# Optimization experiments

Measured on AMD Instinct MI355X. Metric: run time of the kernel, lower is better.

Reference implementation:

```python
import jax, jax.numpy as jnp
import numpy as np
import math

N, IN, OUT, H, EDIM, E = 50000, 128, 64, 2, 64, 1600000
HC = H * OUT
EPS = 1e-16


def segment_softmax(alpha, idx, num_segments):
    # alpha: [E, H], idx: [E] destination node per edge
    m = jax.ops.segment_max(alpha, idx, num_segments=num_segments)  # [N, H]
    m = jnp.where(jnp.isfinite(m), m, 0.0)
    a = jnp.exp(alpha - m[idx])
    s = jax.ops.segment_sum(a, idx, num_segments=num_segments)  # [N, H]
    return a / (s[idx] + EPS)


def setup_inputs() -> dict:
    key = jax.random.key(0)
    ks = jax.random.split(key, 10)
    sx = 1.0 / math.sqrt(IN)
    se = 1.0 / math.sqrt(EDIM)
    x = jax.random.normal(ks[0], (N, IN), dtype=jnp.float32)
    edge_index = jax.random.randint(ks[1], (2, E), 0, N, dtype=jnp.int64)
    edge_attr = jax.random.normal(ks[2], (E, EDIM), dtype=jnp.float32)
    Wq = jax.random.normal(ks[3], (IN, HC), dtype=jnp.float32) * sx
    bq = jnp.zeros((HC,), dtype=jnp.float32)
    Wk = jax.random.normal(ks[4], (IN, HC), dtype=jnp.float32) * sx
    bk = jnp.zeros((HC,), dtype=jnp.float32)
    Wv = jax.random.normal(ks[5], (IN, HC), dtype=jnp.float32) * sx
    bv = jnp.zeros((HC,), dtype=jnp.float32)
    We = jax.random.normal(ks[6], (EDIM, HC), dtype=jnp.float32) * se  # lin_edge, no bias
    Wskip = jax.random.normal(ks[7], (IN, HC), dtype=jnp.float32) * sx
    bskip = jnp.zeros((HC,), dtype=jnp.float32)
    return {"x": x, "edge_index": edge_index, "edge_attr": edge_attr,
            "Wq": Wq, "bq": bq, "Wk": Wk, "bk": bk, "Wv": Wv, "bv": bv,
            "We": We, "Wskip": Wskip, "bskip": bskip}


def reference(x, edge_index, edge_attr, Wq, bq, Wk, bk, Wv, bv, We, Wskip, bskip):
    src, dst = edge_index[0], edge_index[1]  # messages flow src(j) -> dst(i)
    q = (x @ Wq + bq).reshape(N, H, OUT)
    k = (x @ Wk + bk).reshape(N, H, OUT)
    v = (x @ Wv + bv).reshape(N, H, OUT)
    e = (edge_attr @ We).reshape(E, H, OUT)
    k_j = k[src] + e                      # [E, H, C]
    q_i = q[dst]                          # [E, H, C]
    alpha = jnp.sum(q_i * k_j, axis=-1) / math.sqrt(OUT)  # [E, H]
    alpha = segment_softmax(alpha, dst, N)                # dropout=identity (eval)
    msg = (v[src] + e) * alpha[:, :, None]                # [E, H, C]
    out = jax.ops.segment_sum(msg, dst, num_segments=N).reshape(N, HC)
    out = out + x @ Wskip + bskip          # root_weight skip connection
    return out
```

## Files before the change

kernel.cpp:

```cpp
#include <hip/hip_runtime.h>
#include <hip/hip_fp16.h>

constexpr int NN = 50000;
constexpr int EE = 1600000;
constexpr int NB = 196;

typedef __attribute__((ext_vector_type(8))) short bf16x8;
typedef __attribute__((ext_vector_type(4))) float f32x4;

__device__ inline short f2bf(float f) {
    unsigned u = __builtin_bit_cast(unsigned, f);
    u += 0x7fff + ((u >> 16) & 1);
    return (short)(u >> 16);
}

__global__ __launch_bounds__(256) void node_gemm(
    const float* __restrict__ x,
    const float* __restrict__ Wq, const float* __restrict__ bq,
    const float* __restrict__ Wk, const float* __restrict__ bk,
    const float* __restrict__ Wv, const float* __restrict__ bv,
    const float* __restrict__ Ws, const float* __restrict__ bs,
    __half* __restrict__ qt, __half* __restrict__ kt, __half* __restrict__ vt,
    float* __restrict__ skip)
{
    __shared__ short As[64 * 128];
    __shared__ short Bs[128 * 128];
    const int tid = threadIdx.x;
    const int mat = blockIdx.y;
    const float* __restrict__ W    = mat == 0 ? Wq : mat == 1 ? Wk : mat == 2 ? Wv : Ws;
    const float* __restrict__ bias = mat == 0 ? bq : mat == 1 ? bk : mat == 2 ? bv : bs;

    #pragma unroll 4
    for (int idx = tid; idx < 16384; idx += 256) {
        int k = idx >> 7, n = idx & 127;
        int chunk = (k >> 3) ^ (n & 15);
        Bs[n * 128 + chunk * 8 + (k & 7)] = f2bf(W[idx]);
    }
    const int row0 = blockIdx.x * 64;
    #pragma unroll 4
    for (int idx = tid; idx < 8192; idx += 256) {
        int r = idx >> 7, k = idx & 127;
        int node = row0 + r;
        float v = (node < NN) ? x[(size_t)node * 128 + k] : 0.f;
        int chunk = (k >> 3) ^ (r & 15);
        As[r * 128 + chunk * 8 + (k & 7)] = f2bf(v);
    }
    __syncthreads();

    const int wave = tid >> 6, lane = tid & 63;
    const int m16 = lane & 15, quad = lane >> 4;
    const int arow = wave * 16 + m16;
    f32x4 acc[8] = {};
    #pragma unroll
    for (int ks = 0; ks < 4; ks++) {
        int c = ks * 4 + quad;
        bf16x8 af = *(const bf16x8*)&As[arow * 128 + (c ^ (arow & 15)) * 8];
        #pragma unroll
        for (int t = 0; t < 8; t++) {
            int n = t * 16 + m16;
            bf16x8 bf = *(const bf16x8*)&Bs[n * 128 + (c ^ (n & 15)) * 8];
            acc[t] = __builtin_amdgcn_mfma_f32_16x16x32_bf16(af, bf, acc[t], 0, 0, 0);
        }
    }
    __half* __restrict__ T = mat == 0 ? qt : mat == 1 ? kt : vt;
    #pragma unroll
    for (int t = 0; t < 8; t++) {
        int col = t * 16 + m16;
        float bv_ = bias[col];
        #pragma unroll
        for (int r = 0; r < 4; r++) {
            int node = row0 + wave * 16 + quad * 4 + r;
            if (node < NN) {
                float val = acc[t][r] + bv_;
                if (mat < 3)
                    T[node * 128 + (col & 63) * 2 + (col >> 6)] = __float2half(val);
                else
                    skip[node * 128 + col] = val;
            }
        }
    }
}

__global__ __launch_bounds__(256) void edge_gemm(
    const float* __restrict__ ea, const float* __restrict__ We,
    __half* __restrict__ et)
{
    __shared__ short As[64 * 64];
    __shared__ short Bs[128 * 64];
    const int tid = threadIdx.x;
    #pragma unroll 4
    for (int idx = tid; idx < 8192; idx += 256) {
        int k = idx >> 7, n = idx & 127;
        int chunk = (k >> 3) ^ (n & 7);
        Bs[n * 64 + chunk * 8 + (k & 7)] = f2bf(We[idx]);
    }
    const int row0 = blockIdx.x * 64;
    #pragma unroll 4
    for (int idx = tid; idx < 4096; idx += 256) {
        int r = idx >> 6, k = idx & 63;
        int chunk = (k >> 3) ^ (r & 7);
        As[r * 64 + chunk * 8 + (k & 7)] = f2bf(ea[(size_t)(row0 + r) * 64 + k]);
    }
    __syncthreads();

    const int wave = tid >> 6, lane = tid & 63;
    const int m16 = lane & 15, quad = lane >> 4;
    const int arow = wave * 16 + m16;
    f32x4 acc[8] = {};
    #pragma unroll
    for (int ks = 0; ks < 2; ks++) {
        int c = ks * 4 + quad;
        bf16x8 af = *(const bf16x8*)&As[arow * 64 + (c ^ (arow & 7)) * 8];
        #pragma unroll
        for (int t = 0; t < 8; t++) {
            int n = t * 16 + m16;
            bf16x8 bf = *(const bf16x8*)&Bs[n * 64 + (c ^ (n & 7)) * 8];
            acc[t] = __builtin_amdgcn_mfma_f32_16x16x32_bf16(af, bf, acc[t], 0, 0, 0);
        }
    }
    #pragma unroll
    for (int t = 0; t < 8; t++) {
        int col = t * 16 + m16;
        int coff = (col & 63) * 2 + (col >> 6);
        #pragma unroll
        for (int r = 0; r < 4; r++) {
            int edge = row0 + wave * 16 + quad * 4 + r;
            et[(size_t)edge * 128 + coff] = __float2half(acc[t][r]);
        }
    }
}

__global__ void k_hist(const int* __restrict__ dst, int* __restrict__ cnt) {
    int i = blockIdx.x * 256 + threadIdx.x;
    if (i < EE) atomicAdd(&cnt[dst[i]], 1);
}

__global__ __launch_bounds__(256) void k_scan1(const int* __restrict__ cnt,
                                               int* __restrict__ offs,
                                               int* __restrict__ bsum) {
    __shared__ int s[256];
    int t = threadIdx.x, i = blockIdx.x * 256 + t;
    int v = (i < NN) ? cnt[i] : 0;
    s[t] = v; __syncthreads();
    #pragma unroll
    for (int d = 1; d < 256; d <<= 1) {
        int u = (t >= d) ? s[t - d] : 0;
        __syncthreads(); s[t] += u; __syncthreads();
    }
    if (i < NN) offs[i] = s[t] - v;
    if (t == 255) bsum[blockIdx.x] = s[255];
}

__global__ __launch_bounds__(256) void k_scan2(int* __restrict__ bsum) {
    __shared__ int s[256];
    int t = threadIdx.x;
    int v = (t < NB) ? bsum[t] : 0;
    s[t] = v; __syncthreads();
    #pragma unroll
    for (int d = 1; d < 256; d <<= 1) {
        int u = (t >= d) ? s[t - d] : 0;
        __syncthreads(); s[t] += u; __syncthreads();
    }
    if (t < NB) bsum[t] = s[t] - v;
}

__global__ void k_scan3(int* __restrict__ offs, const int* __restrict__ bsum) {
    int i = blockIdx.x * 256 + threadIdx.x;
    if (i < NN) offs[i] += bsum[i >> 8];
    if (i == NN) offs[NN] = EE;
}

__global__ void k_scatter(const int* __restrict__ ei, const int* __restrict__ offs,
                          int* __restrict__ curp, int2* __restrict__ sorted) {
    int i = blockIdx.x * 256 + threadIdx.x;
    if (i >= EE) return;
    int d = ei[EE + i];
    int pos = offs[d] + atomicAdd(&curp[d], 1);
    sorted[pos] = make_int2(ei[i], i);
}

__global__ __launch_bounds__(256) void k_edge(
    const __half2* __restrict__ qt, const __half2* __restrict__ kt,
    const __half2* __restrict__ vt, const __half2* __restrict__ et,
    const int2* __restrict__ sorted, const int* __restrict__ offs,
    const float* __restrict__ skip, float* __restrict__ out)
{
    const int node = blockIdx.x * 4 + (threadIdx.x >> 6);
    const int lane = threadIdx.x & 63;
    if (node >= NN) return;
    const float K2E = 1.4426950408889634f / 8.0f;

    float2 qf = __half22float2(qt[node * 64 + lane]);
    float s0 = 0.f, s1 = 0.f, a0 = 0.f, a1 = 0.f;
    const int beg = offs[node], end = offs[node + 1];

    for (int base = beg; base < end; base += 64) {
        int cnt = min(64, end - base);
        int2 myp = (lane < cnt) ? sorted[base + lane] : make_int2(0, 0);
        for (int i = 0; i < cnt; i++) {
            int src = __shfl(myp.x, i);
            int eid = __shfl(myp.y, i);
            float2 kf = __half22float2(kt[src * 64 + lane]);
            float2 vf = __half22float2(vt[src * 64 + lane]);
            float2 ef = __half22float2(et[(size_t)eid * 64 + lane]);
            float p0 = qf.x * (kf.x + ef.x);
            float p1 = qf.y * (kf.y + ef.y);
            #pragma unroll
            for (int m = 32; m; m >>= 1) {
                p0 += __shfl_xor(p0, m);
                p1 += __shfl_xor(p1, m);
            }
            float al0 = exp2f(p0 * K2E);
            float al1 = exp2f(p1 * K2E);
            s0 += al0; s1 += al1;
            a0 += al0 * (vf.x + ef.x);
            a1 += al1 * (vf.y + ef.y);
        }
    }
    float o0 = a0 / (s0 + 1e-16f) + skip[node * 128 + lane];
    float o1 = a1 / (s1 + 1e-16f) + skip[node * 128 + 64 + lane];
    out[node * 128 + lane] = o0;
    out[node * 128 + 64 + lane] = o1;
}

extern "C" void kernel_launch(void* const* d_in, const int* in_sizes, int n_in,
                              void* d_out, int out_size, void* d_ws, size_t ws_size,
                              hipStream_t stream) {
    const float* x   = (const float*)d_in[0];
    const int*   ei  = (const int*)d_in[1];
    const float* ea  = (const float*)d_in[2];
    const float* Wq  = (const float*)d_in[3];
    const float* bq  = (const float*)d_in[4];
    const float* Wk  = (const float*)d_in[5];
    const float* bk  = (const float*)d_in[6];
    const float* Wv  = (const float*)d_in[7];
    const float* bv  = (const float*)d_in[8];
    const float* We  = (const float*)d_in[9];
    const float* Wsk = (const float*)d_in[10];
    const float* bsk = (const float*)d_in[11];
    float* out = (float*)d_out;

    char* w = (char*)d_ws;
    __half* qt   = (__half*)(w + 0);
    __half* kt   = (__half*)(w + 12800000);
    __half* vt   = (__half*)(w + 25600000);
    float*  skip = (float*)(w + 38400000);
    __half* et   = (__half*)(w + 64000000);
    int2*   sorted = (int2*)(w + 473600000);
    int*    cnt  = (int*)(w + 486400000);
    int*    curp = (int*)(w + 486600000);
    int*    bsum = (int*)(w + 486800000);
    int*    offs = (int*)(w + 486801024);

    (void)hipMemsetAsync(w + 486400000, 0, 401024, stream);

    node_gemm<<<dim3(782, 4), 256, 0, stream>>>(x, Wq, bq, Wk, bk, Wv, bv, Wsk, bsk,
                                                qt, kt, vt, skip);
    edge_gemm<<<25000, 256, 0, stream>>>(ea, We, et);
    k_hist<<<6250, 256, 0, stream>>>(ei + EE, cnt);
    k_scan1<<<NB, 256, 0, stream>>>(cnt, offs, bsum);
    k_scan2<<<1, 256, 0, stream>>>(bsum);
    k_scan3<<<NB, 256, 0, stream>>>(offs, bsum);
    k_scatter<<<6250, 256, 0, stream>>>(ei, offs, curp, sorted);
    k_edge<<<12500, 256, 0, stream>>>((const __half2*)qt, (const __half2*)kt,
                                      (const __half2*)vt, (const __half2*)et,
                                      sorted, offs, skip, out);
}
```

Baseline: 1.168 ms.

## Pre-transpose weights to bf16, interleave K/V, and vectorize edge attention loop

Measured after the change: 1.061 ms. 9.1% less time.

```diff
diff --git a/kernel.cpp b/kernel.cpp
--- a/kernel.cpp
+++ b/kernel.cpp
@@ -7,6 +7,7 @@
 
 typedef __attribute__((ext_vector_type(8))) short bf16x8;
 typedef __attribute__((ext_vector_type(4))) float f32x4;
+typedef _Float16 half2v __attribute__((ext_vector_type(2)));
 
 __device__ inline short f2bf(float f) {
     unsigned u = __builtin_bit_cast(unsigned, f);
@@ -14,36 +15,71 @@
     return (short)(u >> 16);
 }
 
+__device__ inline float fast_exp2(float x) {
+#if __has_builtin(__builtin_amdgcn_exp2f)
+    return __builtin_amdgcn_exp2f(x);
+#else
+    return exp2f(x);
+#endif
+}
+
+__device__ inline float dot2(__half2 a, __half2 b) {
+#if __has_builtin(__builtin_amdgcn_fdot2)
+    return __builtin_amdgcn_fdot2(__builtin_bit_cast(half2v, a),
+                                  __builtin_bit_cast(half2v, b), 0.f, false);
+#else
+    float2 af = __half22float2(a), bf = __half22float2(b);
+    return af.x * bf.x + af.y * bf.y;
+#endif
+}
+
+__global__ void w_conv(const float* __restrict__ Wq, const float* __restrict__ Wk,
+                       const float* __restrict__ Wv, const float* __restrict__ Ws,
+                       const float* __restrict__ We,
+                       short* __restrict__ Wtb, short* __restrict__ Wetb) {
+    int i = blockIdx.x * 256 + threadIdx.x;
+    if (i < 65536) {
+        int mat = i >> 14, n = (i >> 7) & 127, k = i & 127;
+        const float* W = mat == 0 ? Wq : mat == 1 ? Wk : mat == 2 ? Wv : Ws;
+        Wtb[i] = f2bf(W[k * 128 + n]);
+    } else {
+        int j = i - 65536;
+        int n = j >> 6, k = j & 63;
+        Wetb[j] = f2bf(We[k * 128 + n]);
+    }
+}
+
 __global__ __launch_bounds__(256) void node_gemm(
-    const float* __restrict__ x,
-    const float* __restrict__ Wq, const float* __restrict__ bq,
-    const float* __restrict__ Wk, const float* __restrict__ bk,
-    const float* __restrict__ Wv, const float* __restrict__ bv,
-    const float* __restrict__ Ws, const float* __restrict__ bs,
-    __half* __restrict__ qt, __half* __restrict__ kt, __half* __restrict__ vt,
+    const float* __restrict__ x, const short* __restrict__ Wtb,
+    const float* __restrict__ bq, const float* __restrict__ bk,
+    const float* __restrict__ bv, const float* __restrict__ bs,
+    __half2* __restrict__ qt, __half2* __restrict__ kvt,
     float* __restrict__ skip)
 {
     __shared__ short As[64 * 128];
     __shared__ short Bs[128 * 128];
     const int tid = threadIdx.x;
     const int mat = blockIdx.y;
-    const float* __restrict__ W    = mat == 0 ? Wq : mat == 1 ? Wk : mat == 2 ? Wv : Ws;
+    const short* __restrict__ Wt = Wtb + mat * 16384;
     const float* __restrict__ bias = mat == 0 ? bq : mat == 1 ? bk : mat == 2 ? bv : bs;
 
-    #pragma unroll 4
-    for (int idx = tid; idx < 16384; idx += 256) {
-        int k = idx >> 7, n = idx & 127;
-        int chunk = (k >> 3) ^ (n & 15);
-        Bs[n * 128 + chunk * 8 + (k & 7)] = f2bf(W[idx]);
+    #pragma unroll
+    for (int v8 = tid; v8 < 2048; v8 += 256) {
+        int n = v8 >> 4, k8 = v8 & 15;
+        int chunk = k8 ^ (n & 15);
+        *(bf16x8*)&Bs[n * 128 + chunk * 8] = *(const bf16x8*)&Wt[n * 128 + k8 * 8];
     }
     const int row0 = blockIdx.x * 64;
-    #pragma unroll 4
-    for (int idx = tid; idx < 8192; idx += 256) {
-        int r = idx >> 7, k = idx & 127;
+    #pragma unroll
+    for (int v4 = tid; v4 < 2048; v4 += 256) {
+        int r = v4 >> 5, k4 = v4 & 31;
         int node = row0 + r;
-        float v = (node < NN) ? x[(size_t)node * 128 + k] : 0.f;
+        float4 xv = (node < NN) ? *(const float4*)&x[(size_t)node * 128 + k4 * 4]
+                                : make_float4(0.f, 0.f, 0.f, 0.f);
+        int k = k4 * 4;
         int chunk = (k >> 3) ^ (r & 15);
-        As[r * 128 + chunk * 8 + (k & 7)] = f2bf(v);
+        *(short4*)&As[r * 128 + chunk * 8 + (k & 7)] =
+            make_short4(f2bf(xv.x), f2bf(xv.y), f2bf(xv.z), f2bf(xv.w));
     }
     __syncthreads();
 
@@ -62,44 +98,54 @@
             acc[t] = __builtin_amdgcn_mfma_f32_16x16x32_bf16(af, bf, acc[t], 0, 0, 0);
         }
     }
-    __half* __restrict__ T = mat == 0 ? qt : mat == 1 ? kt : vt;
     #pragma unroll
     for (int t = 0; t < 8; t++) {
         int col = t * 16 + m16;
         float bv_ = bias[col];
+        int h = t >> 2;
+        int c2 = (t & 3) * 8 + (m16 >> 1);
+        int hoff = h * 32 + c2;
         #pragma unroll
         for (int r = 0; r < 4; r++) {
             int node = row0 + wave * 16 + quad * 4 + r;
+            float val = acc[t][r] + bv_;
+            float nb = __shfl_xor(val, 1);
             if (node < NN) {
-                float val = acc[t][r] + bv_;
-                if (mat < 3)
-                    T[node * 128 + (col & 63) * 2 + (col >> 6)] = __float2half(val);
-                else
+                if (mat == 3) {
                     skip[node * 128 + col] = val;
+                } else if (!(m16 & 1)) {
+                    __half2 hv = __halves2half2(__float2half(val), __float2half(nb));
+                    if (mat == 0)      qt[node * 64 + hoff] = hv;
+                    else if (mat == 1) kvt[node * 128 + 2 * hoff] = hv;
+                    else               kvt[node * 128 + 2 * hoff + 1] = hv;
+                }
             }
         }
     }
 }
 
 __global__ __launch_bounds__(256) void edge_gemm(
-    const float* __restrict__ ea, const float* __restrict__ We,
-    __half* __restrict__ et)
+    const float* __restrict__ ea, const short* __restrict__ Wetb,
+    __half2* __restrict__ et)
 {
     __shared__ short As[64 * 64];
     __shared__ short Bs[128 * 64];
     const int tid = threadIdx.x;
-    #pragma unroll 4
-    for (int idx = tid; idx < 8192; idx += 256) {
-        int k = idx >> 7, n = idx & 127;
-        int chunk = (k >> 3) ^ (n & 7);
-        Bs[n * 64 + chunk * 8 + (k & 7)] = f2bf(We[idx]);
+    #pragma unroll
+    for (int v8 = tid; v8 < 1024; v8 += 256) {
+        int n = v8 >> 3, k8 = v8 & 7;
+        int chunk = k8 ^ (n & 7);
+        *(bf16x8*)&Bs[n * 64 + chunk * 8] = *(const bf16x8*)&Wetb[n * 64 + k8 * 8];
     }
     const int row0 = blockIdx.x * 64;
-    #pragma unroll 4
-    for (int idx = tid; idx < 4096; idx += 256) {
-        int r = idx >> 6, k = idx & 63;
+    #pragma unroll
+    for (int v4 = tid; v4 < 1024; v4 += 256) {
+        int r = v4 >> 4, k4 = v4 & 15;
+        float4 xv = *(const float4*)&ea[(size_t)(row0 + r) * 64 + k4 * 4];
+        int k = k4 * 4;
         int chunk = (k >> 3) ^ (r & 7);
-        As[r * 64 + chunk * 8 + (k & 7)] = f2bf(ea[(size_t)(row0 + r) * 64 + k]);
+        *(short4*)&As[r * 64 + chunk * 8 + (k & 7)] =
+            make_short4(f2bf(xv.x), f2bf(xv.y), f2bf(xv.z), f2bf(xv.w));
     }
     __syncthreads();
 
@@ -120,12 +166,16 @@
     }
     #pragma unroll
     for (int t = 0; t < 8; t++) {
-        int col = t * 16 + m16;
-        int coff = (col & 63) * 2 + (col >> 6);
+        int h = t >> 2;
+        int hoff = h * 32 + (t & 3) * 8 + (m16 >> 1);
         #pragma unroll
         for (int r = 0; r < 4; r++) {
             int edge = row0 + wave * 16 + quad * 4 + r;
-            et[(size_t)edge * 128 + coff] = __float2half(acc[t][r]);
+            float a = acc[t][r];
+            float b = __shfl_xor(a, 1);
+            if (!(m16 & 1))
+                et[(size_t)edge * 64 + hoff] =
+                    __halves2half2(__float2half(a), __float2half(b));
         }
     }
 }
@@ -180,47 +230,51 @@
 }
 
 __global__ __launch_bounds__(256) void k_edge(
-    const __half2* __restrict__ qt, const __half2* __restrict__ kt,
-    const __half2* __restrict__ vt, const __half2* __restrict__ et,
+    const __half2* __restrict__ qt, const uint2* __restrict__ kvt,
+    const __half2* __restrict__ et,
     const int2* __restrict__ sorted, const int* __restrict__ offs,
-    const float* __restrict__ skip, float* __restrict__ out)
+    const float2* __restrict__ skip, float2* __restrict__ out)
 {
     const int node = blockIdx.x * 4 + (threadIdx.x >> 6);
     const int lane = threadIdx.x & 63;
     if (node >= NN) return;
     const float K2E = 1.4426950408889634f / 8.0f;
-
-    float2 qf = __half22float2(qt[node * 64 + lane]);
-    float s0 = 0.f, s1 = 0.f, a0 = 0.f, a1 = 0.f;
+    const int hoff = (lane >> 5) * 32 + (lane & 31);
+
+    __half2 qh = qt[node * 64 + hoff];
+    float s = 0.f;
+    float2 a = make_float2(0.f, 0.f);
     const int beg = offs[node], end = offs[node + 1];
 
     for (int base = beg; base < end; base += 64) {
         int cnt = min(64, end - base);
         int2 myp = (lane < cnt) ? sorted[base + lane] : make_int2(0, 0);
-        for (int i = 0; i < cnt; i++) {
-            int src = __shfl(myp.x, i);
-            int eid = __shfl(myp.y, i);
-            float2 kf = __half22float2(kt[src * 64 + lane]);
-            float2 vf = __half22float2(vt[src * 64 + lane]);
-            float2 ef = __half22float2(et[(size_t)eid * 64 + lane]);
-            float p0 = qf.x * (kf.x + ef.x);
-            float p1 = qf.y * (kf.y + ef.y);
+        int cnt4 = (cnt + 3) & ~3;
+        for (int i0 = 0; i0 < cnt4; i0 += 4) {
             #pragma unroll
-            for (int m = 32; m; m >>= 1) {
-                p0 += __shfl_xor(p0, m);
-                p1 += __shfl_xor(p1, m);
+            for (int j = 0; j < 4; j++) {
+                int i = i0 + j;
+                int src = __shfl(myp.x, i);
+                int eid = __shfl(myp.y, i);
+                uint2 kv = kvt[src * 64 + hoff];
+                __half2 kh = __builtin_bit_cast(__half2, kv.x);
+                __half2 vh = __builtin_bit_cast(__half2, kv.y);
+                __half2 eh = et[(size_t)eid * 64 + hoff];
+                float p = dot2(qh, __hadd2(kh, eh));
+                #pragma unroll
+                for (int m = 1; m < 32; m <<= 1) p += __shfl_xor(p, m);
+                float al = fast_exp2(p * K2E);
+                al = (i < cnt) ? al : 0.f;
+                s += al;
+                float2 vef = __half22float2(__hadd2(vh, eh));
+                a.x = fmaf(al, vef.x, a.x);
+                a.y = fmaf(al, vef.y, a.y);
             }
-            float al0 = exp2f(p0 * K2E);
-            float al1 = exp2f(p1 * K2E);
-            s0 += al0; s1 += al1;
-            a0 += al0 * (vf.x + ef.x);
-            a1 += al1 * (vf.y + ef.y);
-        }
-    }
-    float o0 = a0 / (s0 + 1e-16f) + skip[node * 128 + lane];
-    float o1 = a1 / (s1 + 1e-16f) + skip[node * 128 + 64 + lane];
-    out[node * 128 + lane] = o0;
-    out[node * 128 + 64 + lane] = o1;
+        }
+    }
+    float inv = 1.f / (s + 1e-16f);
+    float2 sk = skip[node * 64 + hoff];
+    out[node * 64 + hoff] = make_float2(a.x * inv + sk.x, a.y * inv + sk.y);
 }
 
 extern "C" void kernel_launch(void* const* d_in, const int* in_sizes, int n_in,
@@ -241,28 +295,30 @@
     float* out = (float*)d_out;
 
     char* w = (char*)d_ws;
-    __half* qt   = (__half*)(w + 0);
-    __half* kt   = (__half*)(w + 12800000);
-    __half* vt   = (__half*)(w + 25600000);
+    __half2* qt  = (__half2*)(w + 0);
+    __half2* kvt = (__half2*)(w + 12800000);
     float*  skip = (float*)(w + 38400000);
-    __half* et   = (__half*)(w + 64000000);
+    __half2* et  = (__half2*)(w + 64000000);
     int2*   sorted = (int2*)(w + 473600000);
     int*    cnt  = (int*)(w + 486400000);
     int*    curp = (int*)(w + 486600000);
     int*    bsum = (int*)(w + 486800000);
     int*    offs = (int*)(w + 486801024);
+    short*  Wtb  = (short*)(w + 487100000);
+    short*  Wetb = (short*)(w + 487231072);
 
     (void)hipMemsetAsync(w + 486400000, 0, 401024, stream);
 
-    node_gemm<<<dim3(782, 4), 256, 0, stream>>>(x, Wq, bq, Wk, bk, Wv, bv, Wsk, bsk,
-                                                qt, kt, vt, skip);
-    edge_gemm<<<25000, 256, 0, stream>>>(ea, We, et);
+    w_conv<<<288, 256, 0, stream>>>(Wq, Wk, Wv, Wsk, We, Wtb, Wetb);
+    node_gemm<<<dim3(782, 4), 256, 0, stream>>>(x, Wtb, bq, bk, bv, bsk,
+                                                qt, (__half2*)kvt, skip);
+    edge_gemm<<<25000, 256, 0, stream>>>(ea, Wetb, et);
     k_hist<<<6250, 256, 0, stream>>>(ei + EE, cnt);
     k_scan1<<<NB, 256, 0, stream>>>(cnt, offs, bsum);
     k_scan2<<<1, 256, 0, stream>>>(bsum);
     k_scan3<<<NB, 256, 0, stream>>>(offs, bsum);
     k_scatter<<<6250, 256, 0, stream>>>(ei, offs, curp, sorted);
-    k_edge<<<12500, 256, 0, stream>>>((const __half2*)qt, (const __half2*)kt,
-                                      (const __half2*)vt, (const __half2*)et,
-                                      sorted, offs, skip, out);
-}
+    k_edge<<<12500, 256, 0, stream>>>(qt, (const uint2*)kvt, et,
+                                      sorted, offs, (const float2*)skip,
+                                      (float2*)out);
+}
```
